# Optimization experiments

Measured on AMD Instinct MI355X. Metric: run time of the kernel, lower is better.

The kernel has to match this reference:

```python
import jax, jax.numpy as jnp
import numpy as np

QLEN, MLEN, BSZ = 1024, 1024, 2
D_MODEL, N_HEAD, D_HEAD, D_INNER = 1024, 16, 64, 4096
KLEN = QLEN + MLEN
RLEN = KLEN + QLEN
EPS = 1e-12
SCALE = 1.0 / np.sqrt(D_HEAD).astype(np.float32)
STD = 0.02


def gelu(x):
    # OpenAI-GPT tanh-approx gelu used by XLNet
    return 0.5 * x * (1.0 + jnp.tanh(np.sqrt(2.0 / np.pi) * (x + 0.044715 * x ** 3)))


def layer_norm(x, g, b):
    m = jnp.mean(x, axis=-1, keepdims=True)
    v = jnp.mean((x - m) ** 2, axis=-1, keepdims=True)
    return (x - m) * jax.lax.rsqrt(v + EPS) * g + b


def rel_shift(x, klen):
    # x: [qlen, rlen, bsz, n_head] -> [qlen, klen, bsz, n_head]
    q, r, b, n = x.shape
    x = jnp.reshape(x, (r, q, b, n))[1:]
    x = jnp.reshape(x, (q, r - 1, b, n))[:, :klen]
    return x


def setup_inputs() -> dict:
    key = jax.random.key(0)
    ks = jax.random.split(key, 16)
    h = jax.random.normal(ks[0], (QLEN, BSZ, D_MODEL), jnp.float32)
    mems = jax.random.normal(ks[1], (MLEN, BSZ, D_MODEL), jnp.float32)
    r = jax.random.normal(ks[2], (RLEN, BSZ, D_MODEL), jnp.float32)
    # segment one-hot: 1 if query and key segments differ (XLNet convention)
    qseg = jax.random.randint(ks[3], (QLEN, BSZ), 0, 2)
    kseg = jax.random.randint(ks[4], (KLEN, BSZ), 0, 2)
    seg_mat = jax.nn.one_hot((qseg[:, None, :] != kseg[None, :, :]).astype(jnp.int32), 2, dtype=jnp.float32)  # [q,k,b,2]
    # causal mask with mems: query i may attend to key j <= i + MLEN
    i = jnp.arange(QLEN)[:, None]
    j = jnp.arange(KLEN)[None, :]
    attn_mask = (j > i + MLEN).astype(jnp.float32)[:, :, None, None]  # [q,k,1,1]
    wq = jax.random.normal(ks[5], (D_MODEL, N_HEAD, D_HEAD), jnp.float32) * STD
    wk = jax.random.normal(ks[6], (D_MODEL, N_HEAD, D_HEAD), jnp.float32) * STD
    wv = jax.random.normal(ks[7], (D_MODEL, N_HEAD, D_HEAD), jnp.float32) * STD
    wo = jax.random.normal(ks[8], (D_MODEL, N_HEAD, D_HEAD), jnp.float32) * STD
    wr = jax.random.normal(ks[9], (D_MODEL, N_HEAD, D_HEAD), jnp.float32) * STD
    r_w_bias = jnp.zeros((N_HEAD, D_HEAD), jnp.float32)
    r_r_bias = jnp.zeros((N_HEAD, D_HEAD), jnp.float32)
    r_s_bias = jnp.zeros((N_HEAD, D_HEAD), jnp.float32)
    seg_embed = jax.random.normal(ks[10], (2, N_HEAD, D_HEAD), jnp.float32) * STD
    ln_attn_g = jnp.ones((D_MODEL,), jnp.float32)
    ln_attn_b = jnp.zeros((D_MODEL,), jnp.float32)
    w1 = jax.random.normal(ks[11], (D_MODEL, D_INNER), jnp.float32) * STD
    b1 = jnp.zeros((D_INNER,), jnp.float32)
    w2 = jax.random.normal(ks[12], (D_INNER, D_MODEL), jnp.float32) * STD
    b2 = jnp.zeros((D_MODEL,), jnp.float32)
    ln_ff_g = jnp.ones((D_MODEL,), jnp.float32)
    ln_ff_b = jnp.zeros((D_MODEL,), jnp.float32)
    return dict(h=h, mems=mems, r=r, seg_mat=seg_mat, attn_mask=attn_mask,
                wq=wq, wk=wk, wv=wv, wo=wo, wr=wr,
                r_w_bias=r_w_bias, r_r_bias=r_r_bias, r_s_bias=r_s_bias, seg_embed=seg_embed,
                ln_attn_g=ln_attn_g, ln_attn_b=ln_attn_b,
                w1=w1, b1=b1, w2=w2, b2=b2, ln_ff_g=ln_ff_g, ln_ff_b=ln_ff_b)


def reference(h, mems, r, seg_mat, attn_mask, wq, wk, wv, wo, wr,
              r_w_bias, r_r_bias, r_s_bias, seg_embed,
              ln_attn_g, ln_attn_b, w1, b1, w2, b2, ln_ff_g, ln_ff_b):
    # content-stream XLNet relative attention (g=None path) + FFN
    cat = jnp.concatenate([mems, h], axis=0)            # [klen,b,h]
    q_h = jnp.einsum('ibh,hnd->ibnd', h, wq)
    k_h = jnp.einsum('ibh,hnd->ibnd', cat, wk)
    v_h = jnp.einsum('ibh,hnd->ibnd', cat, wv)
    k_r = jnp.einsum('ibh,hnd->ibnd', r, wr)
    ac = jnp.einsum('ibnd,jbnd->ijbn', q_h + r_w_bias, k_h)
    bd = jnp.einsum('ibnd,jbnd->ijbn', q_h + r_r_bias, k_r)
    bd = rel_shift(bd, KLEN)
    ef = jnp.einsum('ibnd,snd->ibns', q_h + r_s_bias, seg_embed)
    ef = jnp.einsum('ijbs,ibns->ijbn', seg_mat, ef)
    attn_score = (ac + bd + ef) * SCALE - 1e30 * attn_mask
    attn_prob = jax.nn.softmax(attn_score, axis=1)
    attn_vec = jnp.einsum('ijbn,jbnd->ibnd', attn_prob, v_h)
    attn_out = jnp.einsum('ibnd,hnd->ibh', attn_vec, wo) + h
    out_h = layer_norm(attn_out, ln_attn_g, ln_attn_b)
    ff = gelu(out_h @ w1 + b1) @ w2 + b2
    return layer_norm(ff + out_h, ln_ff_g, ln_ff_b)
```

## Files before the change

kernel.cpp:

```cpp
#include <hip/hip_runtime.h>
#include <hip/hip_bf16.h>


#define QLEN 1024
#define MLEN 1024
#define DM 1024
#define NH 16
#define DH 64
#define DI 4096
#define KLEN 2048
#define RLEN 3072

typedef __attribute__((ext_vector_type(8))) short s16x8;
typedef __attribute__((ext_vector_type(4))) float f32x4;
typedef unsigned short us;

__device__ __forceinline__ float bf2f(us u) {
    union { unsigned int i; float f; } x; x.i = ((unsigned int)u) << 16; return x.f;
}
__device__ __forceinline__ us f2bf(float f) {
    union { float f; unsigned int i; } x; x.f = f;
    return (us)((x.i + 0x7fffu + ((x.i >> 16) & 1u)) >> 16);
}
__device__ __forceinline__ void gload16(const void* g, void* lds) {
    __builtin_amdgcn_global_load_lds(
        (const __attribute__((address_space(1))) unsigned int*)g,
        (__attribute__((address_space(3))) unsigned int*)lds, 16, 0, 0);
}

template<bool ISMAX>
__device__ __forceinline__ float block_reduce(float v, float* red, int t) {
    #pragma unroll
    for (int off = 32; off > 0; off >>= 1) {
        float o = __shfl_down(v, off);
        v = ISMAX ? fmaxf(v, o) : (v + o);
    }
    if ((t & 63) == 0) red[t >> 6] = v;
    __syncthreads();
    if (t == 0) {
        float s = red[0];
        #pragma unroll
        for (int w = 1; w < 4; ++w) s = ISMAX ? fmaxf(s, red[w]) : (s + red[w]);
        red[4] = s;
    }
    __syncthreads();
    return red[4];
}

__global__ __launch_bounds__(256) void prep_k(
    const float* __restrict__ mems, const float* __restrict__ h,
    const float* __restrict__ r, const float* __restrict__ wo,
    const float* __restrict__ wq, const float* __restrict__ wk,
    const float* __restrict__ wv, const float* __restrict__ wr,
    const float* __restrict__ w1, const float* __restrict__ w2,
    const float* __restrict__ seg,
    us* __restrict__ cat_bf, us* __restrict__ r_bf, us* __restrict__ wo_b,
    us* __restrict__ wqkv_t, us* __restrict__ wr_t,
    us* __restrict__ w1_t, us* __restrict__ w2_t, us* __restrict__ ksb)
{
    __shared__ us tbuf[64][65];
    int bid = blockIdx.x;
    const int tid = threadIdx.x;
    if (bid < 5632) {
        int t = bid * 256 + tid;
        const float* src; us* dst; int off;
        if (t < 262144)       { src = mems; dst = cat_bf;           off = t; }
        else if (t < 524288)  { src = h;    dst = cat_bf + 2097152; off = t - 262144; }
        else if (t < 1310720) { src = r;    dst = r_bf;             off = t - 524288; }
        else                  { src = wo;   dst = wo_b;             off = t - 1310720; }
        const float4* p = (const float4*)src + 2 * (size_t)off;
        float4 a = p[0], b = p[1];
        us o[8] = { f2bf(a.x), f2bf(a.y), f2bf(a.z), f2bf(a.w),
                    f2bf(b.x), f2bf(b.y), f2bf(b.z), f2bf(b.w) };
        *((uint4*)dst + off) = *(const uint4*)o;
        return;
    }
    bid -= 5632;
    if (bid >= 3072) {
        int t = (bid - 3072) * 256 + tid;
        int bb = t >> 11, j = t & 2047;
        ksb[t] = f2bf(seg[(size_t)j * 4 + bb * 2 + 1]);
        return;
    }
    const float* in; us* out; int R, C, c0, r0;
    if (bid < 1024) {
        int z = bid >> 8, u = bid & 255;
        in  = (z == 0) ? wq : (z == 1) ? wk : (z == 2) ? wv : wr;
        out = (z < 3) ? (wqkv_t + (size_t)z * 1048576) : wr_t;
        R = 1024; C = 1024; c0 = (u & 15) * 64; r0 = (u >> 4) * 64;
    } else if (bid < 2048) {
        int u = bid - 1024;
        in = w1; out = w1_t; R = 1024; C = 4096;
        c0 = (u & 63) * 64; r0 = (u >> 6) * 64;
    } else {
        int u = bid - 2048;
        in = w2; out = w2_t; R = 4096; C = 1024;
        c0 = (u & 15) * 64; r0 = (u >> 4) * 64;
    }
    #pragma unroll
    for (int u = 0; u < 16; ++u) {
        int idx = tid + 256 * u;
        int rr = idx >> 6, cc = idx & 63;
        tbuf[cc][rr] = f2bf(in[(size_t)(r0 + rr) * C + c0 + cc]);
    }
    __syncthreads();
    #pragma unroll
    for (int u = 0; u < 16; ++u) {
        int idx = tid + 256 * u;
        int rr = idx >> 6, cc = idx & 63;
        out[(size_t)(c0 + rr) * R + r0 + cc] = tbuf[rr][cc];
    }
}

__device__ __forceinline__ int offe(int r, int c) {
    return ((r >> 4) * 2 + (c >> 5)) * 512 + (r & 15) * 32 + ((c & 31) ^ ((r & 8) ? 16 : 0));
}

template<int EPI>
__device__ __forceinline__ void gemm8h_core(
    const us* __restrict__ A, const us* __restrict__ Bt,
    const float* __restrict__ bias, void* __restrict__ Cout,
    int N, int K, int kbeg, int kchunk, size_t zoff, bool zfirst,
    int bx, int by, us* __restrict__ As8, us* __restrict__ Bs8)
{
    const int tid = threadIdx.x;
    const int w = tid >> 6, l = tid & 63;
    const int lm = l & 15, lg = l >> 4;
    const int wm = w >> 2, wn = w & 3;
    const int m0 = by * 128, n0 = bx * 128;

    int srow[2], scol[2];
    #pragma unroll
    for (int u = 0; u < 2; ++u) {
        int sub = u * 8 + w;
        srow[u] = (sub >> 1) * 16 + (l >> 2);
        scol[u] = (sub & 1) * 32 + (((l & 3) * 8) ^ ((l & 32) ? 16 : 0));
    }

    auto stageHalf = [&](int kt1, bool isB, int u, int db) {
        const us* src = isB ? (Bt + (size_t)n0 * K) : (A + (size_t)m0 * K);
        us* dst = (isB ? Bs8 : As8) + db * 8192 + (u * 8 + w) * 512;
        gload16(src + (size_t)srow[u] * K + kbeg + kt1 * 64 + scol[u], dst);
    };

    f32x4 acc[4][2] = {};
    const int nkt = kchunk / 64;

    stageHalf(0, false, 0, 0); stageHalf(0, false, 1, 0);
    stageHalf(0, true, 0, 0);  stageHalf(0, true, 1, 0);

    for (int kt = 0; kt < nkt; ++kt) {
        const int d = kt & 1;
        asm volatile("s_waitcnt vmcnt(0)" ::: "memory");
        __builtin_amdgcn_s_barrier();
        asm volatile("" ::: "memory");
        const bool hn = (kt + 1 < nkt);
        const us* Ab = As8 + d * 8192;
        const us* Bb = Bs8 + d * 8192;

        if (hn) { stageHalf(kt + 1, false, 0, d ^ 1); stageHalf(kt + 1, true, 0, d ^ 1); }
        s16x8 rB[2][2], rA[2][2];
        #pragma unroll
        for (int nf = 0; nf < 2; ++nf)
            #pragma unroll
            for (int kk = 0; kk < 2; ++kk)
                rB[nf][kk] = *(const s16x8*)&Bb[offe(wn * 32 + nf * 16 + lm, kk * 32 + lg * 8)];
        #pragma unroll
        for (int mf = 0; mf < 2; ++mf)
            #pragma unroll
            for (int kk = 0; kk < 2; ++kk)
                rA[mf][kk] = *(const s16x8*)&Ab[offe(wm * 64 + mf * 16 + lm, kk * 32 + lg * 8)];
        __builtin_amdgcn_s_setprio(1);
        #pragma unroll
        for (int mf = 0; mf < 2; ++mf)
            #pragma unroll
            for (int nf = 0; nf < 2; ++nf)
                #pragma unroll
                for (int kk = 0; kk < 2; ++kk)
                    acc[mf][nf] = __builtin_amdgcn_mfma_f32_16x16x32_bf16(
                        rA[mf][kk], rB[nf][kk], acc[mf][nf], 0, 0, 0);
        __builtin_amdgcn_s_setprio(0);

        if (hn) { stageHalf(kt + 1, false, 1, d ^ 1); stageHalf(kt + 1, true, 1, d ^ 1); }
        #pragma unroll
        for (int mf = 0; mf < 2; ++mf)
            #pragma unroll
            for (int kk = 0; kk < 2; ++kk)
                rA[mf][kk] = *(const s16x8*)&Ab[offe(wm * 64 + (2 + mf) * 16 + lm, kk * 32 + lg * 8)];
        __builtin_amdgcn_s_setprio(1);
        #pragma unroll
        for (int mf = 0; mf < 2; ++mf)
            #pragma unroll
            for (int nf = 0; nf < 2; ++nf)
                #pragma unroll
                for (int kk = 0; kk < 2; ++kk)
                    acc[2 + mf][nf] = __builtin_amdgcn_mfma_f32_16x16x32_bf16(
                        rA[mf][kk], rB[nf][kk], acc[2 + mf][nf], 0, 0, 0);
        __builtin_amdgcn_s_setprio(0);
    }

    #pragma unroll
    for (int mf = 0; mf < 4; ++mf) {
        #pragma unroll
        for (int nf = 0; nf < 2; ++nf) {
            #pragma unroll
            for (int rr = 0; rr < 4; ++rr) {
                int row = m0 + wm * 64 + mf * 16 + lg * 4 + rr;
                int col = n0 + wn * 32 + nf * 16 + lm;
                float v = acc[mf][nf][rr];
                if (EPI == 1 || (EPI == 2 && zfirst)) v += bias[col];
                if (EPI == 1) {
                    float targ = 0.7978845608028654f * (v + 0.044715f * v * v * v);
                    v = 0.5f * v * (1.0f + tanhf(targ));
                    ((us*)Cout)[(size_t)row * N + col] = f2bf(v);
                } else if (EPI == 2) {
                    ((float*)Cout + zoff)[(size_t)row * N + col] = v;
                } else if (EPI == 3) {
                    int s = row >> 1, bb = row & 1, nn = col >> 6, dd = col & 63;
                    if (s >= 1) {
                        int g = (s - 1) >> 4, lmw = (s - 1) & 15;
                        int ks2 = dd >> 5, lg2 = (dd >> 3) & 3, e2 = dd & 7;
                        ((us*)Cout)[((((size_t)(bb * 16 + nn)) * 144 + g) * 2 + ks2) * 512
                                    + (lg2 * 16 + lmw) * 8 + e2] = f2bf(v);
                    }
                } else {
                    int which = col >> 10;
                    int nn = (col >> 6) & 15, dd = col & 63, bb = row & 1;
                    us val = f2bf(v);
                    us* base = (us*)Cout;
                    if (which == 0) {
                        if (row >= 2048)
                            base[(((size_t)(bb * 16 + nn)) * 1024 + ((row - 2048) >> 1)) * 64 + dd] = val;
                    } else if (which == 1) {
                        int j = row >> 1;
                        int jt = j >> 6, ff = (j >> 4) & 3, lmw = j & 15;
                        int ks2 = dd >> 5, lg2 = (dd >> 3) & 3, e2 = dd & 7;
                        (base + 2097152)[((((size_t)(bb * 16 + nn)) * 32 + jt) * 8 + ff * 2 + ks2) * 512
                                         + (lg2 * 16 + lmw) * 8 + e2] = val;
                    } else {
                        int j = row >> 1;
                        int jt = j >> 6, ks2 = (j >> 5) & 1, lg2 = (j >> 3) & 3, e2 = j & 7;
                        int df = dd >> 4, lmw = dd & 15;
                        (base + 6291456)[((((size_t)(bb * 16 + nn)) * 32 + jt) * 8 + df * 2 + ks2) * 512
                                         + (lg2 * 16 + lmw) * 8 + e2] = val;
                    }
                }
            }
        }
    }
}

__global__ __launch_bounds__(512, 4) void proj8_k(
    const us* __restrict__ cat_bf, const us* __restrict__ wqkv_t,
    const us* __restrict__ r_bf, const us* __restrict__ wr_t,
    us* __restrict__ qkv_out, us* __restrict__ krf_out)
{
    __shared__ __align__(16) us As8[2 * 8192];
    __shared__ __align__(16) us Bs8[2 * 8192];
    int bid = blockIdx.x;
    if (bid < 768) {
        int swz = (bid & 7) * 96 + (bid >> 3);
        gemm8h_core<4>(cat_bf, wqkv_t, nullptr, qkv_out, 3072, 1024, 0, 1024,
                       0, true, swz % 24, swz / 24, As8, Bs8);
    } else {
        int idx = bid - 768;
        int swz = (idx & 7) * 34 + (idx >> 3);
        gemm8h_core<3>(r_bf, wr_t, nullptr, krf_out, 1024, 1024, 0, 1024,
                       0, true, swz % 8, swz / 8, As8, Bs8);
    }
}

template<int EPI>
__global__ __launch_bounds__(512, 4) void gemm8f_k(
    const us* __restrict__ A, const us* __restrict__ Bt,
    const float* __restrict__ bias, void* __restrict__ Cout,
    int N, int K, int kchunk, size_t zstride)
{
    __shared__ __align__(16) us As8[2 * 8192];
    __shared__ __align__(16) us Bs8[2 * 8192];
    int lin = blockIdx.y * gridDim.x + blockIdx.x;
    int nwg = gridDim.x * gridDim.y;
    int swz = (lin & 7) * (nwg >> 3) + (lin >> 3);
    int bx = swz % gridDim.x, by = swz / gridDim.x;
    gemm8h_core<EPI>(A, Bt, bias, Cout, N, K, blockIdx.z * kchunk, kchunk,
                     (size_t)blockIdx.z * zstride, blockIdx.z == 0, bx, by, As8, Bs8);
}

template<int TM, int EPI>
__device__ __forceinline__ void gemm_core(
    const us* __restrict__ A, const us* __restrict__ Bt,
    const float* __restrict__ bias, void* __restrict__ Cout,
    int N, int K, int kbeg, int kchunk, size_t zoff, bool zfirst,
    int bx, int by, us* __restrict__ As, us* __restrict__ Bs)
{
    constexpr int MF = TM / 32;
    constexpr int AISS = TM / 64;
    const int tid = threadIdx.x;
    const int w = tid >> 6, l = tid & 63;
    const int lm = l & 15, lg = l >> 4;
    const int m0 = by * TM, n0 = bx * 128;
    const int wr = (w >> 1) * (TM / 2), wc = (w & 1) * 64;
    const int nt = kchunk / 32;

    f32x4 acc[MF][4] = {};

    auto stage = [&](int buf, int k0) {
        #pragma unroll
        for (int u = 0; u < AISS; ++u) {
            int c = (u * 4 + w) * 64 + l;
            int row = c & (TM - 1), kc = c >> (TM == 128 ? 7 : 6);
            gload16(A + (size_t)(m0 + row) * K + k0 + kc * 8,
                    As + buf * (TM * 32) + (u * 4 + w) * 512);
        }
        #pragma unroll
        for (int u = 0; u < 2; ++u) {
            int c = (u * 4 + w) * 64 + l;
            int row = c & 127, kc = c >> 7;
            gload16(Bt + (size_t)(n0 + row) * K + k0 + kc * 8,
                    Bs + buf * 4096 + (u * 4 + w) * 512);
        }
    };

    stage(0, kbeg);
    int cur = 0;
    for (int t = 0; t < nt; ++t) {
        asm volatile("s_waitcnt vmcnt(0)" ::: "memory");
        __builtin_amdgcn_s_barrier();
        asm volatile("" ::: "memory");
        if (t + 1 < nt) stage(cur ^ 1, kbeg + (t + 1) * 32);

        s16x8 af[MF], bfr[4];
        #pragma unroll
        for (int mf = 0; mf < MF; ++mf)
            af[mf] = *(const s16x8*)&As[cur * (TM * 32) + (lg * TM + wr + mf * 16 + lm) * 8];
        #pragma unroll
        for (int nf = 0; nf < 4; ++nf)
            bfr[nf] = *(const s16x8*)&Bs[cur * 4096 + (lg * 128 + wc + nf * 16 + lm) * 8];
        #pragma unroll
        for (int mf = 0; mf < MF; ++mf)
            #pragma unroll
            for (int nf = 0; nf < 4; ++nf)
                acc[mf][nf] = __builtin_amdgcn_mfma_f32_16x16x32_bf16(
                    af[mf], bfr[nf], acc[mf][nf], 0, 0, 0);
        cur ^= 1;
    }

    #pragma unroll
    for (int mf = 0; mf < MF; ++mf) {
        #pragma unroll
        for (int nf = 0; nf < 4; ++nf) {
            #pragma unroll
            for (int rr = 0; rr < 4; ++rr) {
                int row = m0 + wr + mf * 16 + lg * 4 + rr;
                int col = n0 + wc + nf * 16 + lm;
                float v = acc[mf][nf][rr];
                if (EPI == 2 && zfirst) v += bias[col];
                ((float*)Cout + zoff)[(size_t)row * N + col] = v;
            }
        }
    }
}

template<int TM, int EPI>
__global__ __launch_bounds__(256) void gemm2(
    const us* __restrict__ A, const us* __restrict__ Bt,
    const float* __restrict__ bias, void* __restrict__ Cout,
    int N, int K, int kchunk, size_t zstride)
{
    __shared__ us As[2 * TM * 32];
    __shared__ us Bs[2 * 128 * 32];
    int lin = blockIdx.y * gridDim.x + blockIdx.x;
    int nwg = gridDim.x * gridDim.y;
    int swz = (lin & 7) * (nwg >> 3) + (lin >> 3);
    int bx = swz % gridDim.x, by = swz / gridDim.x;
    gemm_core<TM, EPI>(A, Bt, bias, Cout, N, K, blockIdx.z * kchunk, kchunk,
                       (size_t)blockIdx.z * zstride, blockIdx.z == 0, bx, by, As, Bs);
}

__global__ __launch_bounds__(256) void attn11_k(
    const us* __restrict__ qb, const us* __restrict__ kfr, const us* __restrict__ vfr,
    const us* __restrict__ krf, const us* __restrict__ ksb,
    const float* __restrict__ rwb, const float* __restrict__ rrb,
    const float* __restrict__ rsb, const float* __restrict__ se,
    const float* __restrict__ seg,
    float* __restrict__ po, float* __restrict__ pm, float* __restrict__ pl)
{
    __shared__ float G_lds[4 * 80 * 20];
    __shared__ us P_lds[4 * 16 * 64];
    __shared__ us KS_lds[2048];
    __shared__ float Qx_lds[64][2];

    const int tid = threadIdx.x;
    const int w = tid >> 6, l = tid & 63;
    const int lm = l & 15, lg = l >> 4;
    int lin = blockIdx.x;
    const int half = lin >> 9;
    const int i0t = (lin >> 5) & 15;
    const int bn = lin & 31;
    const int i0 = i0t * 64;
    const int b = bn >> 4, n = bn & 15;
    const int i = i0 + w * 16 + lm;

    const float SC = 0.125f * 1.44269504088896340736f;

    const us* kbase = kfr + (size_t)bn * 131072;
    const us* vbase = vfr + (size_t)bn * 131072;
    const us* krbase = krf + (size_t)bn * 147456;

    gload16(ksb + b * KLEN + (w * 64 + l) * 8, &KS_lds[w * 512]);
    {
        const us* qrow = qb + ((size_t)bn * QLEN + i0 + l) * DH;
        s16x8 qv8[8];
        #pragma unroll
        for (int c = 0; c < 8; ++c) qv8[c] = *(const s16x8*)(qrow + c * 8);
        float e0 = 0.f, e1 = 0.f;
        #pragma unroll
        for (int c = 0; c < 8; ++c)
            #pragma unroll
            for (int e = 0; e < 8; ++e) {
                int d = c * 8 + e;
                float qv = bf2f((us)qv8[c][e]) + rsb[n * DH + d];
                e0 = fmaf(qv, se[(0 * NH + n) * DH + d], e0);
                e1 = fmaf(qv, se[(1 * NH + n) * DH + d], e1);
            }
        float qsI = seg[(size_t)(i0 + l) * 8192 + b * 2 + 1];
        float qs0 = seg[b * 2 + 1];
        float qs = (qsI != qs0) ? 1.f : 0.f;
        float ed = e1 - e0;
        if (w == 0) {
            Qx_lds[l][0] = (e0 + qs * ed) * SC;
            Qx_lds[l][1] = ed * (1.f - 2.f * qs) * SC;
        }
    }
    asm volatile("s_waitcnt vmcnt(0)" ::: "memory");
    __syncthreads();

    s16x8 qwf[2], qrf[2], qxf;
    {
        const us* qrow = qb + ((size_t)bn * QLEN + i) * DH;
        #pragma unroll
        for (int ks = 0; ks < 2; ++ks) {
            s16x8 v = *(const s16x8*)(qrow + ks * 32 + lg * 8);
            #pragma unroll
            for (int e = 0; e < 8; ++e) {
                int d = ks * 32 + lg * 8 + e;
                float f = bf2f((us)v[e]);
                qwf[ks][e] = (short)f2bf((f + rwb[n * DH + d]) * SC);
                qrf[ks][e] = (short)f2bf((f + rrb[n * DH + d]) * SC);
            }
        }
        #pragma unroll
        for (int e = 0; e < 8; ++e) qxf[e] = 0;
        if (lg == 0) {
            qxf[0] = (short)f2bf(Qx_lds[w * 16 + lm][0]);
            qxf[1] = (short)f2bf(Qx_lds[w * 16 + lm][1]);
        }
    }

    int njt = ((i0 + 63 + MLEN) >> 6) + 1;
    if (njt > 32) njt = 32;
    const int nj0 = (njt + 1) >> 1;
    const int jbeg = half ? nj0 : 0;
    const int jend = half ? njt : nj0;
    const int gq = 63 - (i0 >> 4) - w;

    f32x4 of[4] = {{0,0,0,0},{0,0,0,0},{0,0,0,0},{0,0,0,0}};
    float M = -3.0e38f, L = 0.f;
    float* gw = &G_lds[w * 1600];
    us* pw = &P_lds[w * 1024];

    for (int jt = jbeg; jt < jend; ++jt) {
        const int j0 = jt * 64;

        s16x8 kf[4][2], vf[4][2];
        #pragma unroll
        for (int f = 0; f < 4; ++f) {
            #pragma unroll
            for (int ks = 0; ks < 2; ++ks) {
                kf[f][ks] = *(const s16x8*)(kbase + (size_t)(((jt * 4 + f) * 2 + ks) * 64 + l) * 8);
                vf[f][ks] = *(const s16x8*)(vbase + (size_t)(((jt * 4 + f) * 2 + ks) * 64 + l) * 8);
            }
        }

        __builtin_amdgcn_s_setprio(1);
        #pragma unroll
        for (int pf = 0; pf < 5; ++pf) {
            int g = gq + 4 * jt + pf;
            f32x4 gacc = {0, 0, 0, 0};
            #pragma unroll
            for (int ks = 0; ks < 2; ++ks) {
                s16x8 a = *(const s16x8*)(krbase + (size_t)((g * 2 + ks) * 64 + l) * 8);
                gacc = __builtin_amdgcn_mfma_f32_16x16x32_bf16(a, qrf[ks], gacc, 0, 0, 0);
            }
            #pragma unroll
            for (int rr = 0; rr < 4; ++rr)
                gw[(pf * 16 + lg * 4 + rr) * 20 + lm] = gacc[rr];
        }
        f32x4 sf[4];
        #pragma unroll
        for (int f = 0; f < 4; ++f) {
            f32x4 cfr = {0, 0, 0, 0};
            cfr = __builtin_amdgcn_mfma_f32_16x16x32_bf16(kf[f][0], qwf[0], cfr, 0, 0, 0);
            cfr = __builtin_amdgcn_mfma_f32_16x16x32_bf16(kf[f][1], qwf[1], cfr, 0, 0, 0);
            s16x8 aext;
            #pragma unroll
            for (int e = 0; e < 8; ++e) aext[e] = 0;
            if (lg == 0) {
                aext[0] = (short)0x3F80;
                aext[1] = (short)KS_lds[j0 + f * 16 + lm];
            }
            cfr = __builtin_amdgcn_mfma_f32_16x16x32_bf16(aext, qxf, cfr, 0, 0, 0);
            sf[f] = cfr;
        }
        __builtin_amdgcn_s_setprio(0);

        float sv[16];
        #pragma unroll
        for (int f = 0; f < 4; ++f)
            #pragma unroll
            for (int rr = 0; rr < 4; ++rr) {
                int jl = f * 16 + lg * 4 + rr;
                sv[f * 4 + rr] = sf[f][rr] + gw[(jl + 15 - lm) * 20 + lm];
            }
        if (j0 + 63 > i0 + w * 16 + MLEN) {
            #pragma unroll
            for (int f = 0; f < 4; ++f)
                #pragma unroll
                for (int rr = 0; rr < 4; ++rr) {
                    int jl = f * 16 + lg * 4 + rr;
                    if (j0 + jl > i + MLEN) sv[f * 4 + rr] = -1.0e30f;
                }
        }
        float tmax = sv[0];
        #pragma unroll
        for (int u = 1; u < 16; ++u) tmax = fmaxf(tmax, sv[u]);
        tmax = fmaxf(tmax, __shfl_xor(tmax, 16));
        tmax = fmaxf(tmax, __shfl_xor(tmax, 32));
        float Mnew = fmaxf(M, tmax);
        float scale;
        asm("v_exp_f32 %0, %1" : "=v"(scale) : "v"(M - Mnew));
        float psum = 0.f;
        unsigned int pk[8];
        #pragma unroll
        for (int f = 0; f < 4; ++f) {
            #pragma unroll
            for (int rp = 0; rp < 2; ++rp) {
                float p0, p1;
                asm("v_exp_f32 %0, %1" : "=v"(p0) : "v"(sv[f * 4 + rp * 2] - Mnew));
                asm("v_exp_f32 %0, %1" : "=v"(p1) : "v"(sv[f * 4 + rp * 2 + 1] - Mnew));
                psum += p0 + p1;
                unsigned int pkv;
                asm("v_cvt_pk_bf16_f32 %0, %1, %2" : "=v"(pkv) : "v"(p0), "v"(p1));
                pk[f * 2 + rp] = pkv;
            }
        }
        psum += __shfl_xor(psum, 16);
        psum += __shfl_xor(psum, 32);
        L = L * scale + psum;
        M = Mnew;
        float rs4[4];
        #pragma unroll
        for (int rr = 0; rr < 4; ++rr)
            rs4[rr] = __shfl(scale, (l & 48) | (lg * 4 + rr));
        #pragma unroll
        for (int df = 0; df < 4; ++df)
            #pragma unroll
            for (int rr = 0; rr < 4; ++rr)
                of[df][rr] *= rs4[rr];
        #pragma unroll
        for (int f = 0; f < 4; ++f) {
            #pragma unroll
            for (int rp = 0; rp < 2; ++rp) {
                int jl2 = f * 16 + lg * 4 + rp * 2;
                *(unsigned int*)&pw[lm * 64 + (((jl2 * 2) ^ ((lm & 7) << 4)) >> 1)] = pk[f * 2 + rp];
            }
        }
        __builtin_amdgcn_s_setprio(1);
        #pragma unroll
        for (int ks = 0; ks < 2; ++ks) {
            s16x8 pa = *(const s16x8*)&pw[lm * 64 + (((ks * 64 + lg * 16) ^ ((lm & 7) << 4)) >> 1)];
            #pragma unroll
            for (int df = 0; df < 4; ++df)
                of[df] = __builtin_amdgcn_mfma_f32_16x16x32_bf16(pa, vf[df][ks], of[df], 0, 0, 0);
        }
        __builtin_amdgcn_s_setprio(0);
    }

    const int pidx = (half * 16 + i0t) * 32 + bn;
    float rl4[4], rm4[4];
    #pragma unroll
    for (int rr = 0; rr < 4; ++rr) {
        rl4[rr] = __shfl(L, (l & 48) | (lg * 4 + rr));
        rm4[rr] = __shfl(M, (l & 48) | (lg * 4 + rr));
    }
    #pragma unroll
    for (int df = 0; df < 4; ++df) {
        #pragma unroll
        for (int rr = 0; rr < 4; ++rr) {
            int rloc = w * 16 + lg * 4 + rr;
            po[((size_t)pidx * 64 + rloc) * 64 + df * 16 + lm] = of[df][rr];
        }
    }
    if (lm == 0) {
        #pragma unroll
        for (int rr = 0; rr < 4; ++rr) {
            int rloc = w * 16 + lg * 4 + rr;
            pm[pidx * 64 + rloc] = rm4[rr];
            pl[pidx * 64 + rloc] = rl4[rr];
        }
    }
}

__global__ __launch_bounds__(256) void avcomb_k(
    const float* __restrict__ po, const float* __restrict__ pm,
    const float* __restrict__ pl, us* __restrict__ av)
{
    const int avrow = blockIdx.x;
    const int t = threadIdx.x;
    const int i = avrow >> 1, b = avrow & 1;
    const int i0t = i >> 6, rl = i & 63;
    const int col0 = t * 4;
    const int n = col0 >> 6, d0 = col0 & 63;
    const int bn = b * 16 + n;
    const int p0 = (0 + i0t) * 32 + bn;
    const int p1 = (16 + i0t) * 32 + bn;
    float M0 = pm[p0 * 64 + rl], M1 = pm[p1 * 64 + rl];
    float L0 = pl[p0 * 64 + rl], L1 = pl[p1 * 64 + rl];
    float Mx = fmaxf(M0, M1);
    float s0, s1;
    asm("v_exp_f32 %0, %1" : "=v"(s0) : "v"(M0 - Mx));
    asm("v_exp_f32 %0, %1" : "=v"(s1) : "v"(M1 - Mx));
    float inv = 1.0f / (L0 * s0 + L1 * s1);
    float4 o0 = *(const float4*)&po[((size_t)p0 * 64 + rl) * 64 + d0];
    float4 o1 = *(const float4*)&po[((size_t)p1 * 64 + rl) * 64 + d0];
    us o[4] = { f2bf((o0.x * s0 + o1.x * s1) * inv),
                f2bf((o0.y * s0 + o1.y * s1) * inv),
                f2bf((o0.z * s0 + o1.z * s1) * inv),
                f2bf((o0.w * s0 + o1.w * s1) * inv) };
    *(unsigned long long*)&av[(size_t)avrow * 1024 + col0] = *(const unsigned long long*)o;
}

template<int NSUM, bool RESBF, bool OUTBF>
__global__ __launch_bounds__(256) void ln_k(
    const float* __restrict__ a, const void* __restrict__ resid,
    const float* __restrict__ g, const float* __restrict__ bb,
    void* __restrict__ out)
{
    __shared__ float xs[DM];
    __shared__ float red[5];
    const int r = blockIdx.x;
    const int t = threadIdx.x;
    float lsum = 0.f;
    #pragma unroll
    for (int u = 0; u < 4; ++u) {
        int hdx = t + 256 * u;
        float x = RESBF ? bf2f(((const us*)resid)[(size_t)r * DM + hdx])
                        : ((const float*)resid)[(size_t)r * DM + hdx];
        #pragma unroll
        for (int s = 0; s < NSUM; ++s)
            x += a[(size_t)s * 2097152 + (size_t)r * DM + hdx];
        xs[hdx] = x;
        lsum += x;
    }
    float m = block_reduce<false>(lsum, red, t) * (1.0f / DM);
    float lv = 0.f;
    #pragma unroll
    for (int u = 0; u < 4; ++u) {
        int hdx = t + 256 * u;
        float dd = xs[hdx] - m;
        lv += dd * dd;
    }
    float var = block_reduce<false>(lv, red, t) * (1.0f / DM);
    float rs = rsqrtf(var + 1e-12f);
    #pragma unroll
    for (int u = 0; u < 4; ++u) {
        int hdx = t + 256 * u;
        float y = (xs[hdx] - m) * rs * g[hdx] + bb[hdx];
        if (OUTBF) ((us*)out)[(size_t)r * DM + hdx] = f2bf(y);
        else       ((float*)out)[(size_t)r * DM + hdx] = y;
    }
}

extern "C" void kernel_launch(void* const* d_in, const int* in_sizes, int n_in,
                              void* d_out, int out_size, void* d_ws, size_t ws_size,
                              hipStream_t stream) {
    const float* h         = (const float*)d_in[0];
    const float* mems      = (const float*)d_in[1];
    const float* r         = (const float*)d_in[2];
    const float* seg_mat   = (const float*)d_in[3];
    const float* wq        = (const float*)d_in[5];
    const float* wk        = (const float*)d_in[6];
    const float* wv        = (const float*)d_in[7];
    const float* wo        = (const float*)d_in[8];
    const float* wr        = (const float*)d_in[9];
    const float* rwb       = (const float*)d_in[10];
    const float* rrb       = (const float*)d_in[11];
    const float* rsb       = (const float*)d_in[12];
    const float* seg_embed = (const float*)d_in[13];
    const float* ln_g      = (const float*)d_in[14];
    const float* ln_b      = (const float*)d_in[15];
    const float* w1        = (const float*)d_in[16];
    const float* b1        = (const float*)d_in[17];
    const float* w2        = (const float*)d_in[18];
    const float* b2        = (const float*)d_in[19];
    const float* lf_g      = (const float*)d_in[20];
    const float* lf_b      = (const float*)d_in[21];
    float* out = (float*)d_out;
    char* W = (char*)d_ws;
    const size_t MB = 1ull << 20;

    us*    cat_bf = (us*)(W);
    us*    r_bf   = (us*)(W + 8  * MB);
    us*    wqkv_t = (us*)(W + 20 * MB);
    us*    wr_t   = (us*)(W + 26 * MB);
    us*    wo_b   = (us*)(W + 28 * MB);
    us*    w1_t   = (us*)(W + 30 * MB);
    us*    w2_t   = (us*)(W + 38 * MB);
    us*    q_bf   = (us*)(W + 46 * MB);
    us*    kfrag  = q_bf + 2097152;
    us*    vfrag  = q_bf + 6291456;
    us*    krf    = (us*)(W + 66 * MB);
    us*    av_bf  = (us*)(W + 78 * MB);
    us*    ks_bf  = (us*)(W + 82 * MB);
    us*    oh_bf  = (us*)(W + 83 * MB);
    float* po     = (float*)(W + 8 * MB);
    float* pm     = (float*)(W + 24 * MB);
    float* pl     = (float*)(W + 24 * MB + 512 * 1024);
    float* ao     = (float*)(W + 8 * MB);
    us*    ff1_bf = (us*)(W + 46 * MB);
    float* ff2    = (float*)(W);

    dim3 blk(256);
    dim3 blk8(512);
    prep_k<<<dim3(8720), blk, 0, stream>>>(mems, h, r, wo, wq, wk, wv, wr, w1, w2, seg_mat,
                                           cat_bf, r_bf, wo_b, wqkv_t, wr_t, w1_t, w2_t, ks_bf);
    proj8_k<<<dim3(1040), blk8, 0, stream>>>(cat_bf, wqkv_t, r_bf, wr_t, q_bf, krf);
    attn11_k<<<dim3(1024), blk, 0, stream>>>(q_bf, kfrag, vfrag, krf, ks_bf,
                                             rwb, rrb, rsb, seg_embed, seg_mat, po, pm, pl);
    avcomb_k<<<dim3(2048), blk, 0, stream>>>(po, pm, pl, av_bf);
    gemm2<64, 0><<<dim3(8, 32, 2), blk, 0, stream>>>(av_bf, wo_b, nullptr, ao, 1024, 1024, 512, 2097152);
    ln_k<2, false, true><<<dim3(2048), blk, 0, stream>>>(ao, h, ln_g, ln_b, oh_bf);
    gemm8f_k<1><<<dim3(32, 16), blk8, 0, stream>>>(oh_bf, w1_t, b1, ff1_bf, 4096, 1024, 1024, 0);
    gemm8f_k<2><<<dim3(8, 16, 4), blk8, 0, stream>>>(ff1_bf, w2_t, b2, ff2, 1024, 4096, 1024, 2097152);
    ln_k<4, true, false><<<dim3(2048), blk, 0, stream>>>(ff2, oh_bf, lf_g, lf_b, out);
}
```

Before: 247.6 us.

## Split attention KV range into four parts and store partials in bf16

The attention kernel now splits each query tile's key range into four parts instead of two, doubling the grid to 2048 workgroups for better occupancy and load balance. Partial outputs are stored as bf16 instead of fp32, which halves partial-output traffic, and the combine kernel merges four partials with log-sum-exp rescaling. The cost is more combine work and more per-block Q setup overhead, plus some precision loss in the partial accumulators.

```diff
diff --git a/kernel.cpp b/kernel.cpp
--- a/kernel.cpp
+++ b/kernel.cpp
@@ -383,7 +383,7 @@
     const float* __restrict__ rwb, const float* __restrict__ rrb,
     const float* __restrict__ rsb, const float* __restrict__ se,
     const float* __restrict__ seg,
-    float* __restrict__ po, float* __restrict__ pm, float* __restrict__ pl)
+    us* __restrict__ po, float* __restrict__ pm, float* __restrict__ pl)
 {
     __shared__ float G_lds[4 * 80 * 20];
     __shared__ us P_lds[4 * 16 * 64];
@@ -394,7 +394,7 @@
     const int w = tid >> 6, l = tid & 63;
     const int lm = l & 15, lg = l >> 4;
     int lin = blockIdx.x;
-    const int half = lin >> 9;
+    const int quarter = lin >> 9;
     const int i0t = (lin >> 5) & 15;
     const int bn = lin & 31;
     const int i0 = i0t * 64;
@@ -459,9 +459,8 @@
 
     int njt = ((i0 + 63 + MLEN) >> 6) + 1;
     if (njt > 32) njt = 32;
-    const int nj0 = (njt + 1) >> 1;
-    const int jbeg = half ? nj0 : 0;
-    const int jend = half ? njt : nj0;
+    const int jbeg = (njt * quarter) >> 2;
+    const int jend = (njt * (quarter + 1)) >> 2;
     const int gq = 63 - (i0 >> 4) - w;
 
     f32x4 of[4] = {{0,0,0,0},{0,0,0,0},{0,0,0,0},{0,0,0,0}};
@@ -586,7 +585,7 @@
         __builtin_amdgcn_s_setprio(0);
     }
 
-    const int pidx = (half * 16 + i0t) * 32 + bn;
+    const int pidx = (quarter * 16 + i0t) * 32 + bn;
     float rl4[4], rm4[4];
     #pragma unroll
     for (int rr = 0; rr < 4; ++rr) {
@@ -598,7 +597,7 @@
         #pragma unroll
         for (int rr = 0; rr < 4; ++rr) {
             int rloc = w * 16 + lg * 4 + rr;
-            po[((size_t)pidx * 64 + rloc) * 64 + df * 16 + lm] = of[df][rr];
+            po[((size_t)pidx * 64 + rloc) * 64 + df * 16 + lm] = f2bf(of[df][rr]);
         }
     }
     if (lm == 0) {
@@ -612,7 +611,7 @@
 }
 
 __global__ __launch_bounds__(256) void avcomb_k(
-    const float* __restrict__ po, const float* __restrict__ pm,
+    const us* __restrict__ po, const float* __restrict__ pm,
     const float* __restrict__ pl, us* __restrict__ av)
 {
     const int avrow = blockIdx.x;
@@ -622,21 +621,34 @@
     const int col0 = t * 4;
     const int n = col0 >> 6, d0 = col0 & 63;
     const int bn = b * 16 + n;
-    const int p0 = (0 + i0t) * 32 + bn;
-    const int p1 = (16 + i0t) * 32 + bn;
-    float M0 = pm[p0 * 64 + rl], M1 = pm[p1 * 64 + rl];
-    float L0 = pl[p0 * 64 + rl], L1 = pl[p1 * 64 + rl];
-    float Mx = fmaxf(M0, M1);
-    float s0, s1;
-    asm("v_exp_f32 %0, %1" : "=v"(s0) : "v"(M0 - Mx));
-    asm("v_exp_f32 %0, %1" : "=v"(s1) : "v"(M1 - Mx));
-    float inv = 1.0f / (L0 * s0 + L1 * s1);
-    float4 o0 = *(const float4*)&po[((size_t)p0 * 64 + rl) * 64 + d0];
-    float4 o1 = *(const float4*)&po[((size_t)p1 * 64 + rl) * 64 + d0];
-    us o[4] = { f2bf((o0.x * s0 + o1.x * s1) * inv),
-                f2bf((o0.y * s0 + o1.y * s1) * inv),
-                f2bf((o0.z * s0 + o1.z * s1) * inv),
-                f2bf((o0.w * s0 + o1.w * s1) * inv) };
+    int pq[4];
+    float Mq[4], Lq[4];
+    float Mx = -3.0e38f;
+    #pragma unroll
+    for (int q = 0; q < 4; ++q) {
+        pq[q] = (q * 16 + i0t) * 32 + bn;
+        Mq[q] = pm[pq[q] * 64 + rl];
+        Lq[q] = pl[pq[q] * 64 + rl];
+        Mx = fmaxf(Mx, Mq[q]);
+    }
+    float sq[4], den = 0.f;
+    #pragma unroll
+    for (int q = 0; q < 4; ++q) {
+        asm("v_exp_f32 %0, %1" : "=v"(sq[q]) : "v"(Mq[q] - Mx));
+        den += Lq[q] * sq[q];
+    }
+    float inv = 1.0f / den;
+    float acc[4] = {0.f, 0.f, 0.f, 0.f};
+    #pragma unroll
+    for (int q = 0; q < 4; ++q) {
+        unsigned long long pk = *(const unsigned long long*)
+            &po[((size_t)pq[q] * 64 + rl) * 64 + d0];
+        #pragma unroll
+        for (int e = 0; e < 4; ++e)
+            acc[e] = fmaf(bf2f((us)(pk >> (16 * e))), sq[q], acc[e]);
+    }
+    us o[4] = { f2bf(acc[0] * inv), f2bf(acc[1] * inv),
+                f2bf(acc[2] * inv), f2bf(acc[3] * inv) };
     *(unsigned long long*)&av[(size_t)avrow * 1024 + col0] = *(const unsigned long long*)o;
 }
 
@@ -723,9 +735,9 @@
     us*    av_bf  = (us*)(W + 78 * MB);
     us*    ks_bf  = (us*)(W + 82 * MB);
     us*    oh_bf  = (us*)(W + 83 * MB);
-    float* po     = (float*)(W + 8 * MB);
-    float* pm     = (float*)(W + 24 * MB);
-    float* pl     = (float*)(W + 24 * MB + 512 * 1024);
+    us*    po     = (us*)(W);
+    float* pm     = (float*)(W + 16 * MB);
+    float* pl     = (float*)(W + 17 * MB);
     float* ao     = (float*)(W + 8 * MB);
     us*    ff1_bf = (us*)(W + 46 * MB);
     float* ff2    = (float*)(W);
@@ -735,7 +747,7 @@
     prep_k<<<dim3(8720), blk, 0, stream>>>(mems, h, r, wo, wq, wk, wv, wr, w1, w2, seg_mat,
                                            cat_bf, r_bf, wo_b, wqkv_t, wr_t, w1_t, w2_t, ks_bf);
     proj8_k<<<dim3(1040), blk8, 0, stream>>>(cat_bf, wqkv_t, r_bf, wr_t, q_bf, krf);
-    attn11_k<<<dim3(1024), blk, 0, stream>>>(q_bf, kfrag, vfrag, krf, ks_bf,
+    attn11_k<<<dim3(2048), blk, 0, stream>>>(q_bf, kfrag, vfrag, krf, ks_bf,
                                              rwb, rrb, rsb, seg_embed, seg_mat, po, pm, pl);
     avcomb_k<<<dim3(2048), blk, 0, stream>>>(po, pm, pl, av_bf);
     gemm2<64, 0><<<dim3(8, 32, 2), blk, 0, stream>>>(av_bf, wo_b, nullptr, ao, 1024, 1024, 512, 2097152);
```

Measured after the change: 274.8 us. 11.0% more time.
